# Kernel optimization log

Measured on AMD Instinct MI355X. Metric: run time of the kernel, lower is better.

The kernel has to match this reference:

```python
import jax, jax.numpy as jnp
import numpy as np

DIM = 1024
CTX_DIM = 1024
HEADS = 16
HEAD_DIM = DIM // HEADS


def setup_inputs() -> dict:
    key = jax.random.key(0)
    ks = jax.random.split(key, 6)
    B, N, M = 2, 2048, 2048
    s = 0.02
    return {
        "x": jax.random.normal(ks[0], (B, N, DIM), dtype=jnp.float32),
        "context": jax.random.normal(ks[1], (B, M, CTX_DIM), dtype=jnp.float32),
        "W_q": jax.random.normal(ks[2], (DIM, DIM), dtype=jnp.float32) * s,
        "W_kv": jax.random.normal(ks[3], (CTX_DIM * 2, CTX_DIM), dtype=jnp.float32) * s,
        "W_proj": jax.random.normal(ks[4], (DIM, DIM), dtype=jnp.float32) * s,
        "b_proj": jax.random.normal(ks[5], (DIM,), dtype=jnp.float32) * s,
    }


def reference(x, context, W_q, W_kv, W_proj, b_proj):
    B, N, C = x.shape
    M = context.shape[1]
    scale = HEAD_DIM ** (-0.5)
    # q projection: [B,N,H,D]
    q = (x @ W_q.T).reshape(B, N, HEADS, HEAD_DIM) * scale
    # context kv projection: [B,M,2,H,D]
    kv = (context @ W_kv.T).reshape(B, M, 2, HEADS, HEAD_DIM)
    k = kv[:, :, 0]  # [B,M,H,D]
    v = kv[:, :, 0]  # NOTE: source uses qkv_context[0] for BOTH k and v (faithful)
    attn = jnp.einsum("bnhd,bmhd->bhnm", q, k)
    attn = jax.nn.softmax(attn, axis=-1)
    out = jnp.einsum("bhnm,bmhd->bnhd", attn, v).reshape(B, N, C)
    return out @ W_proj.T + b_proj
```

## Files before the change

### kernel.cpp

```cpp
#include <hip/hip_runtime.h>
#include <hip/hip_bf16.h>


typedef __bf16 bf16x8 __attribute__((ext_vector_type(8)));
typedef float f32x4 __attribute__((ext_vector_type(4)));
typedef float f32x16 __attribute__((ext_vector_type(16)));

static constexpr int kDIM = 1024;
static constexpr float kLog2e = 1.4426950408889634f;

__device__ inline unsigned short f2bf(float f) {
    union { float f; unsigned int u; } v; v.f = f;
    return (unsigned short)((v.u + 0x7FFFu + ((v.u >> 16) & 1u)) >> 16);
}

__device__ inline unsigned int cvtpk2bf(float a, float b) {
    unsigned int r;
    asm("v_cvt_pk_bf16_f32 %0, %1, %2" : "=v"(r) : "v"(a), "v"(b));
    return r;
}

__device__ inline void gload_lds16(const unsigned short* g, unsigned short* l) {
    __builtin_amdgcn_global_load_lds(
        (const __attribute__((address_space(1))) unsigned int*)g,
        (__attribute__((address_space(3))) unsigned int*)l, 16, 0, 0);
}

__global__ __launch_bounds__(256) void cast_all(
    const float* __restrict__ x, const float* __restrict__ ctx,
    const float* __restrict__ wq, const float* __restrict__ wkv,
    const float* __restrict__ wp,
    unsigned short* __restrict__ xb, unsigned short* __restrict__ cb,
    unsigned short* __restrict__ wqb, unsigned short* __restrict__ wkb,
    unsigned short* __restrict__ wpb)
{
    int j = blockIdx.x * 256 + threadIdx.x;
    const float* s; unsigned short* d;
    if (j < 1048576)                      { s = x;   d = xb;  }
    else if ((j -= 1048576) < 1048576)    { s = ctx; d = cb;  }
    else if ((j -= 1048576) < 262144)     { s = wq;  d = wqb; }
    else if ((j -= 262144) < 262144)      { s = wkv; d = wkb; }
    else if ((j -= 262144) < 262144)      { s = wp;  d = wpb; }
    else return;
    float4 f = ((const float4*)s)[j];
    ushort4 o;
    o.x = f2bf(f.x); o.y = f2bf(f.y); o.z = f2bf(f.z); o.w = f2bf(f.w);
    ((ushort4*)d)[j] = o;
}

__global__ __launch_bounds__(512, 4) void gemm_qk(
    const unsigned short* __restrict__ xb, const unsigned short* __restrict__ cb,
    const unsigned short* __restrict__ Wq, const unsigned short* __restrict__ Wkv,
    unsigned short* __restrict__ Qb, unsigned short* __restrict__ Kb,
    unsigned short* __restrict__ Ktb, float qscale, int Mctx)
{
    __shared__ unsigned short As[128 * 64];
    __shared__ unsigned short Bs[128 * 64];
    const int z = blockIdx.z;
    const unsigned short* A  = z ? cb : xb;
    const unsigned short* Bw = z ? Wkv : Wq;
    unsigned short* Cb = z ? Kb : Qb;
    const float scale = z ? 1.0f : qscale;

    const int tid = threadIdx.x;
    const int wave = tid >> 6, lane = tid & 63;
    const int g = lane >> 4, c = lane & 15;
    const int wm = (wave >> 2) * 64, wn = (wave & 3) * 32;
    const int bm = blockIdx.y * 128, bn = blockIdx.x * 128;

    const int srow = lane >> 3;
    const int scolsw = ((lane & 7) ^ (srow & 7)) * 8;
    const int x7 = c & 7;

    f32x4 acc[4][2];
    #pragma unroll
    for (int i = 0; i < 4; ++i)
        #pragma unroll
        for (int j = 0; j < 2; ++j)
            acc[i][j] = (f32x4){0.f, 0.f, 0.f, 0.f};

    for (int k0 = 0; k0 < kDIM; k0 += 64) {
        __syncthreads();
        #pragma unroll
        for (int t = 0; t < 2; ++t) {
            const int chunk = wave * 2 + t;
            gload_lds16(A + (size_t)(bm + chunk * 8 + srow) * kDIM + k0 + scolsw,
                        &As[chunk * 512]);
        }
        #pragma unroll
        for (int t = 0; t < 2; ++t) {
            const int chunk = wave * 2 + t;
            gload_lds16(Bw + (size_t)(bn + chunk * 8 + srow) * kDIM + k0 + scolsw,
                        &Bs[chunk * 512]);
        }
        __syncthreads();
        #pragma unroll
        for (int kc = 0; kc < 2; ++kc) {
            bf16x8 af[4], bfr[2];
            #pragma unroll
            for (int i = 0; i < 4; ++i)
                af[i] = *(const bf16x8*)&As[(wm + i * 16 + c) * 64 +
                                            ((kc * 4 + g) ^ x7) * 8];
            #pragma unroll
            for (int j = 0; j < 2; ++j)
                bfr[j] = *(const bf16x8*)&Bs[(wn + j * 16 + c) * 64 +
                                             ((kc * 4 + g) ^ x7) * 8];
            #pragma unroll
            for (int i = 0; i < 4; ++i)
                #pragma unroll
                for (int j = 0; j < 2; ++j)
                    acc[i][j] = __builtin_amdgcn_mfma_f32_16x16x32_bf16(
                        af[i], bfr[j], acc[i][j], 0, 0, 0);
        }
    }

    #pragma unroll
    for (int i = 0; i < 4; ++i) {
        #pragma unroll
        for (int j = 0; j < 2; ++j) {
            const int r0 = bm + wm + i * 16 + 4 * g;
            const int cc = bn + wn + j * 16 + c;
            float v0 = acc[i][j][0] * scale;
            float v1 = acc[i][j][1] * scale;
            float v2 = acc[i][j][2] * scale;
            float v3 = acc[i][j][3] * scale;
            Cb[(size_t)(r0 + 0) * kDIM + cc] = f2bf(v0);
            Cb[(size_t)(r0 + 1) * kDIM + cc] = f2bf(v1);
            Cb[(size_t)(r0 + 2) * kDIM + cc] = f2bf(v2);
            Cb[(size_t)(r0 + 3) * kDIM + cc] = f2bf(v3);
            if (z) {
                const int bb = r0 / Mctx, n0 = r0 % Mctx;
                const int hh = cc >> 6, d = cc & 63;
                ushort4 pk;
                pk.x = f2bf(v0); pk.y = f2bf(v1); pk.z = f2bf(v2); pk.w = f2bf(v3);
                *(ushort4*)&Ktb[((size_t)((bb * 16 + hh) * 64 + d)) * Mctx + n0] = pk;
            }
        }
    }
}

__global__ __launch_bounds__(256, 4) void gemm_proj(
    const unsigned short* __restrict__ Ab, const unsigned short* __restrict__ Wp,
    const float* __restrict__ bias, float* __restrict__ out)
{
    __shared__ unsigned short As[64 * 64];
    __shared__ unsigned short Bs[64 * 64];
    const int tid = threadIdx.x;
    const int wave = tid >> 6, lane = tid & 63;
    const int g = lane >> 4, c = lane & 15;
    const int wm = (wave & 1) * 32, wn = (wave >> 1) * 32;
    const int bm = blockIdx.y * 64, bn = blockIdx.x * 64;

    const int srow = lane >> 3;
    const int scolsw = ((lane & 7) ^ (srow & 7)) * 8;
    const int x7 = c & 7;

    f32x4 acc[2][2];
    #pragma unroll
    for (int i = 0; i < 2; ++i)
        #pragma unroll
        for (int j = 0; j < 2; ++j)
            acc[i][j] = (f32x4){0.f, 0.f, 0.f, 0.f};

    for (int k0 = 0; k0 < kDIM; k0 += 64) {
        __syncthreads();
        #pragma unroll
        for (int t = 0; t < 2; ++t) {
            const int chunk = wave * 2 + t;
            const int row = chunk * 8 + srow;
            gload_lds16(Ab + (size_t)(bm + row) * kDIM + k0 + scolsw, &As[chunk * 512]);
            gload_lds16(Wp + (size_t)(bn + row) * kDIM + k0 + scolsw, &Bs[chunk * 512]);
        }
        __syncthreads();
        #pragma unroll
        for (int kc = 0; kc < 2; ++kc) {
            bf16x8 af[2], bfr[2];
            #pragma unroll
            for (int i = 0; i < 2; ++i)
                af[i] = *(const bf16x8*)&As[(wm + i * 16 + c) * 64 +
                                            ((kc * 4 + g) ^ x7) * 8];
            #pragma unroll
            for (int j = 0; j < 2; ++j)
                bfr[j] = *(const bf16x8*)&Bs[(wn + j * 16 + c) * 64 +
                                             ((kc * 4 + g) ^ x7) * 8];
            #pragma unroll
            for (int i = 0; i < 2; ++i)
                #pragma unroll
                for (int j = 0; j < 2; ++j)
                    acc[i][j] = __builtin_amdgcn_mfma_f32_16x16x32_bf16(
                        af[i], bfr[j], acc[i][j], 0, 0, 0);
        }
    }

    #pragma unroll
    for (int i = 0; i < 2; ++i) {
        #pragma unroll
        for (int j = 0; j < 2; ++j) {
            const int r0 = bm + wm + i * 16 + 4 * g;
            const int cc = bn + wn + j * 16 + c;
            const float bv = bias[cc];
            #pragma unroll
            for (int ii = 0; ii < 4; ++ii)
                out[(size_t)(r0 + ii) * kDIM + cc] = acc[i][j][ii] + bv;
        }
    }
}

__global__ __launch_bounds__(512, 4) void attn_mfma_v8(
    const unsigned short* __restrict__ Q,
    const unsigned short* __restrict__ K,
    const unsigned short* __restrict__ Kt,
    unsigned short* __restrict__ O, int N, int M)
{
    __shared__ unsigned short smem[18432];
    unsigned short* Ks  = smem;
    unsigned short* Kts = smem + 64 * 72;

    const int lin  = blockIdx.x + 16 * (blockIdx.y + 16 * blockIdx.z);
    const int orig = (lin & 7) * 64 + (lin >> 3);
    const int q0 = (orig & 15) * 128;
    const int h  = (orig >> 4) & 15;
    const int b  = orig >> 8;

    const int tid = threadIdx.x;
    const int w = tid >> 6, lane = tid & 63;
    const int strip = w >> 1, kh = w & 1;
    const int ql = lane & 31, l5 = lane >> 5;

    const unsigned short* Qrow = Q + (size_t)(b * N + q0 + strip * 32 + ql) * kDIM + h * 64;
    const unsigned short* Kb = K + (size_t)b * M * kDIM + h * 64;
    const unsigned short* Ktb = Kt + (size_t)((b * 16 + h) * 64) * M;

    bf16x8 bq[4];
    #pragma unroll
    for (int kc = 0; kc < 4; ++kc)
        bq[kc] = *(const bf16x8*)(Qrow + kc * 16 + l5 * 8);

    f32x16 ot[2];
    #pragma unroll
    for (int dt = 0; dt < 2; ++dt)
        #pragma unroll
        for (int r = 0; r < 16; ++r) ot[dt][r] = 0.f;
    float lac = 0.f;

    const int srow = tid >> 3, scol = (tid & 7) * 8;

    uint4 rk  = *(const uint4*)(Kb  + (size_t)srow * kDIM + scol);
    uint4 rkt = *(const uint4*)(Ktb + (size_t)srow * M + scol);

    for (int k0 = 0; k0 < M; k0 += 64) {
        __syncthreads();
        *(uint4*)&Ks[srow * 72 + scol]  = rk;
        *(uint4*)&Kts[srow * 72 + scol] = rkt;
        __syncthreads();

        if (k0 + 64 < M) {
            rk  = *(const uint4*)(Kb  + (size_t)(k0 + 64 + srow) * kDIM + scol);
            rkt = *(const uint4*)(Ktb + (size_t)srow * M + (k0 + 64) + scol);
        }

        f32x16 st;
        #pragma unroll
        for (int r = 0; r < 16; ++r) st[r] = 0.f;
        #pragma unroll
        for (int kc = 0; kc < 4; ++kc) {
            bf16x8 ak = *(const bf16x8*)&Ks[(kh * 32 + ql) * 72 + kc * 16 + l5 * 8];
            st = __builtin_amdgcn_mfma_f32_32x32x16_bf16(ak, bq[kc], st, 0, 0, 0);
        }

        float pr[16];
        #pragma unroll
        for (int r = 0; r < 16; ++r) {
            pr[r] = __builtin_amdgcn_exp2f(st[r]);
            lac += pr[r];
        }
        unsigned int dw[8];
        #pragma unroll
        for (int p = 0; p < 8; ++p) dw[p] = cvtpk2bf(pr[2 * p], pr[2 * p + 1]);

        auto s02 = __builtin_amdgcn_permlane32_swap(dw[0], dw[2], false, false);
        auto s13 = __builtin_amdgcn_permlane32_swap(dw[1], dw[3], false, false);
        auto s46 = __builtin_amdgcn_permlane32_swap(dw[4], dw[6], false, false);
        auto s57 = __builtin_amdgcn_permlane32_swap(dw[5], dw[7], false, false);
        union BP { unsigned int u[4]; bf16x8 v; };
        BP b0, b1;
        b0.u[0] = s02[0]; b0.u[1] = s13[0]; b0.u[2] = s02[1]; b0.u[3] = s13[1];
        b1.u[0] = s46[0]; b1.u[1] = s57[0]; b1.u[2] = s46[1]; b1.u[3] = s57[1];
        bf16x8 bp[2] = { b0.v, b1.v };

        #pragma unroll
        for (int kc2 = 0; kc2 < 2; ++kc2) {
            #pragma unroll
            for (int dt = 0; dt < 2; ++dt) {
                bf16x8 av = *(const bf16x8*)&Kts[(dt * 32 + ql) * 72 + kh * 32 + kc2 * 16 + l5 * 8];
                ot[dt] = __builtin_amdgcn_mfma_f32_32x32x16_bf16(av, bp[kc2], ot[dt], 0, 0, 0);
            }
        }
    }

    float lw = lac + __shfl_xor(lac, 32);
    float* Om = (float*)smem;
    float* Lm = Om + 128 * 68;
    const int qi = strip * 32 + ql;

    __syncthreads();
    if (kh == 1) {
        #pragma unroll
        for (int dt = 0; dt < 2; ++dt)
            #pragma unroll
            for (int rr = 0; rr < 4; ++rr)
                *(f32x4*)&Om[qi * 68 + dt * 32 + 8 * rr + 4 * l5] =
                    (f32x4){ot[dt][4 * rr], ot[dt][4 * rr + 1],
                            ot[dt][4 * rr + 2], ot[dt][4 * rr + 3]};
        if (l5 == 0) Lm[qi] = lw;
    }
    __syncthreads();
    if (kh == 0) {
        const float inv = 1.0f / (lw + Lm[qi]);
        unsigned short* Ob = O + (size_t)(b * N + q0 + qi) * kDIM + h * 64;
        #pragma unroll
        for (int dt = 0; dt < 2; ++dt)
            #pragma unroll
            for (int rr = 0; rr < 4; ++rr) {
                f32x4 pv = *(const f32x4*)&Om[qi * 68 + dt * 32 + 8 * rr + 4 * l5];
                ushort4 u;
                u.x = f2bf((ot[dt][4 * rr]     + pv[0]) * inv);
                u.y = f2bf((ot[dt][4 * rr + 1] + pv[1]) * inv);
                u.z = f2bf((ot[dt][4 * rr + 2] + pv[2]) * inv);
                u.w = f2bf((ot[dt][4 * rr + 3] + pv[3]) * inv);
                *(ushort4*)(Ob + dt * 32 + 8 * rr + 4 * l5) = u;
            }
    }
}

extern "C" void kernel_launch(void* const* d_in, const int* in_sizes, int n_in,
                              void* d_out, int out_size, void* d_ws, size_t ws_size,
                              hipStream_t stream)
{
    const float* x      = (const float*)d_in[0];
    const float* ctxp   = (const float*)d_in[1];
    const float* W_q    = (const float*)d_in[2];
    const float* W_kv   = (const float*)d_in[3];
    const float* W_proj = (const float*)d_in[4];
    const float* b_proj = (const float*)d_in[5];
    float* out = (float*)d_out;

    const int B = 2, N = 2048, M = 2048;
    const int BN = B * N;
    const int SQ = kDIM * kDIM;

    unsigned short* p = (unsigned short*)d_ws;
    unsigned short* xb  = p; p += (size_t)BN * kDIM;
    unsigned short* cb  = p; p += (size_t)BN * kDIM;
    unsigned short* wqb = p; p += SQ;
    unsigned short* wkb = p; p += SQ;
    unsigned short* wpb = p; p += SQ;
    unsigned short* Qb  = p; p += (size_t)BN * kDIM;
    unsigned short* Kb  = p; p += (size_t)BN * kDIM;
    unsigned short* Ktb = p; p += (size_t)BN * kDIM;
    unsigned short* Ab  = xb;

    hipLaunchKernelGGL(cast_all, dim3(11264), dim3(256), 0, stream,
                       x, ctxp, W_q, W_kv, W_proj, xb, cb, wqb, wkb, wpb);
    hipLaunchKernelGGL(gemm_qk, dim3(kDIM / 128, BN / 128, 2), dim3(512), 0, stream,
                       xb, cb, wqb, wkb, Qb, Kb, Ktb, 0.125f * kLog2e, M);
    hipLaunchKernelGGL(attn_mfma_v8, dim3(N / 128, 16, B), dim3(512), 0, stream,
                       Qb, Kb, Ktb, Ab, N, M);
    hipLaunchKernelGGL(gemm_proj, dim3(kDIM / 64, BN / 64), dim3(256), 0, stream,
                       Ab, wpb, b_proj, out);
}
```

Before: 177.8 us.

## Double-buffer LDS tiles in GEMMs and attention to overlap loads with MFMA

Both GEMM kernels now use two LDS buffers: the global-to-LDS load for the next k-tile is issued before computing the current one, which leaves one barrier per iteration instead of two. The attention kernel ping-pongs K and K-transpose tiles across two halves of its shared memory, and the register prefetch now runs two tiles ahead. The aim is to hide load latency behind matrix math and reduce synchronisation. The cost is double the LDS footprint in the GEMMs, which can lower occupancy, plus a possible race because the async global_load_lds writes are only ordered by the barrier at the end of the iteration.

```diff
diff --git a/kernel.cpp b/kernel.cpp
--- a/kernel.cpp
+++ b/kernel.cpp
@@ -54,8 +54,8 @@
     unsigned short* __restrict__ Qb, unsigned short* __restrict__ Kb,
     unsigned short* __restrict__ Ktb, float qscale, int Mctx)
 {
-    __shared__ unsigned short As[128 * 64];
-    __shared__ unsigned short Bs[128 * 64];
+    __shared__ unsigned short As[2 * 128 * 64];
+    __shared__ unsigned short Bs[2 * 128 * 64];
     const int z = blockIdx.z;
     const unsigned short* A  = z ? cb : xb;
     const unsigned short* Bw = z ? Wkv : Wq;
@@ -79,31 +79,41 @@
         for (int j = 0; j < 2; ++j)
             acc[i][j] = (f32x4){0.f, 0.f, 0.f, 0.f};
 
-    for (int k0 = 0; k0 < kDIM; k0 += 64) {
-        __syncthreads();
+    auto stage = [&](int buf, int k0) {
+        unsigned short* Ad = As + buf * 8192;
+        unsigned short* Bd = Bs + buf * 8192;
         #pragma unroll
         for (int t = 0; t < 2; ++t) {
             const int chunk = wave * 2 + t;
             gload_lds16(A + (size_t)(bm + chunk * 8 + srow) * kDIM + k0 + scolsw,
-                        &As[chunk * 512]);
+                        Ad + chunk * 512);
         }
         #pragma unroll
         for (int t = 0; t < 2; ++t) {
             const int chunk = wave * 2 + t;
             gload_lds16(Bw + (size_t)(bn + chunk * 8 + srow) * kDIM + k0 + scolsw,
-                        &Bs[chunk * 512]);
-        }
-        __syncthreads();
+                        Bd + chunk * 512);
+        }
+    };
+
+    stage(0, 0);
+    __syncthreads();
+
+    for (int t = 0; t < 16; ++t) {
+        const int cur = t & 1;
+        if (t < 15) stage(cur ^ 1, (t + 1) * 64);
+        const unsigned short* Ac = As + cur * 8192;
+        const unsigned short* Bc = Bs + cur * 8192;
         #pragma unroll
         for (int kc = 0; kc < 2; ++kc) {
             bf16x8 af[4], bfr[2];
             #pragma unroll
             for (int i = 0; i < 4; ++i)
-                af[i] = *(const bf16x8*)&As[(wm + i * 16 + c) * 64 +
+                af[i] = *(const bf16x8*)&Ac[(wm + i * 16 + c) * 64 +
                                             ((kc * 4 + g) ^ x7) * 8];
             #pragma unroll
             for (int j = 0; j < 2; ++j)
-                bfr[j] = *(const bf16x8*)&Bs[(wn + j * 16 + c) * 64 +
+                bfr[j] = *(const bf16x8*)&Bc[(wn + j * 16 + c) * 64 +
                                              ((kc * 4 + g) ^ x7) * 8];
             #pragma unroll
             for (int i = 0; i < 4; ++i)
@@ -112,6 +122,7 @@
                     acc[i][j] = __builtin_amdgcn_mfma_f32_16x16x32_bf16(
                         af[i], bfr[j], acc[i][j], 0, 0, 0);
         }
+        __syncthreads();
     }
 
     #pragma unroll
@@ -143,8 +154,8 @@
     const unsigned short* __restrict__ Ab, const unsigned short* __restrict__ Wp,
     const float* __restrict__ bias, float* __restrict__ out)
 {
-    __shared__ unsigned short As[64 * 64];
-    __shared__ unsigned short Bs[64 * 64];
+    __shared__ unsigned short As[2 * 64 * 64];
+    __shared__ unsigned short Bs[2 * 64 * 64];
     const int tid = threadIdx.x;
     const int wave = tid >> 6, lane = tid & 63;
     const int g = lane >> 4, c = lane & 15;
@@ -162,26 +173,36 @@
         for (int j = 0; j < 2; ++j)
             acc[i][j] = (f32x4){0.f, 0.f, 0.f, 0.f};
 
-    for (int k0 = 0; k0 < kDIM; k0 += 64) {
-        __syncthreads();
+    auto stage = [&](int buf, int k0) {
+        unsigned short* Ad = As + buf * 4096;
+        unsigned short* Bd = Bs + buf * 4096;
         #pragma unroll
         for (int t = 0; t < 2; ++t) {
             const int chunk = wave * 2 + t;
             const int row = chunk * 8 + srow;
-            gload_lds16(Ab + (size_t)(bm + row) * kDIM + k0 + scolsw, &As[chunk * 512]);
-            gload_lds16(Wp + (size_t)(bn + row) * kDIM + k0 + scolsw, &Bs[chunk * 512]);
-        }
-        __syncthreads();
+            gload_lds16(Ab + (size_t)(bm + row) * kDIM + k0 + scolsw, Ad + chunk * 512);
+            gload_lds16(Wp + (size_t)(bn + row) * kDIM + k0 + scolsw, Bd + chunk * 512);
+        }
+    };
+
+    stage(0, 0);
+    __syncthreads();
+
+    for (int t = 0; t < 16; ++t) {
+        const int cur = t & 1;
+        if (t < 15) stage(cur ^ 1, (t + 1) * 64);
+        const unsigned short* Ac = As + cur * 4096;
+        const unsigned short* Bc = Bs + cur * 4096;
         #pragma unroll
         for (int kc = 0; kc < 2; ++kc) {
             bf16x8 af[2], bfr[2];
             #pragma unroll
             for (int i = 0; i < 2; ++i)
-                af[i] = *(const bf16x8*)&As[(wm + i * 16 + c) * 64 +
+                af[i] = *(const bf16x8*)&Ac[(wm + i * 16 + c) * 64 +
                                             ((kc * 4 + g) ^ x7) * 8];
             #pragma unroll
             for (int j = 0; j < 2; ++j)
-                bfr[j] = *(const bf16x8*)&Bs[(wn + j * 16 + c) * 64 +
+                bfr[j] = *(const bf16x8*)&Bc[(wn + j * 16 + c) * 64 +
                                              ((kc * 4 + g) ^ x7) * 8];
             #pragma unroll
             for (int i = 0; i < 2; ++i)
@@ -190,6 +211,7 @@
                     acc[i][j] = __builtin_amdgcn_mfma_f32_16x16x32_bf16(
                         af[i], bfr[j], acc[i][j], 0, 0, 0);
         }
+        __syncthreads();
     }
 
     #pragma unroll
@@ -206,15 +228,13 @@
     }
 }
 
-__global__ __launch_bounds__(512, 4) void attn_mfma_v8(
+__global__ __launch_bounds__(512, 4) void attn_mfma_v9(
     const unsigned short* __restrict__ Q,
     const unsigned short* __restrict__ K,
     const unsigned short* __restrict__ Kt,
     unsigned short* __restrict__ O, int N, int M)
 {
     __shared__ unsigned short smem[18432];
-    unsigned short* Ks  = smem;
-    unsigned short* Kts = smem + 64 * 72;
 
     const int lin  = blockIdx.x + 16 * (blockIdx.y + 16 * blockIdx.z);
     const int orig = (lin & 7) * 64 + (lin >> 3);
@@ -244,19 +264,29 @@
     float lac = 0.f;
 
     const int srow = tid >> 3, scol = (tid & 7) * 8;
+    const int NT = M / 64;
 
     uint4 rk  = *(const uint4*)(Kb  + (size_t)srow * kDIM + scol);
     uint4 rkt = *(const uint4*)(Ktb + (size_t)srow * M + scol);
-
-    for (int k0 = 0; k0 < M; k0 += 64) {
-        __syncthreads();
-        *(uint4*)&Ks[srow * 72 + scol]  = rk;
-        *(uint4*)&Kts[srow * 72 + scol] = rkt;
-        __syncthreads();
-
-        if (k0 + 64 < M) {
-            rk  = *(const uint4*)(Kb  + (size_t)(k0 + 64 + srow) * kDIM + scol);
-            rkt = *(const uint4*)(Ktb + (size_t)srow * M + (k0 + 64) + scol);
+    *(uint4*)&smem[srow * 72 + scol]        = rk;
+    *(uint4*)&smem[4608 + srow * 72 + scol] = rkt;
+    rk  = *(const uint4*)(Kb  + (size_t)(64 + srow) * kDIM + scol);
+    rkt = *(const uint4*)(Ktb + (size_t)srow * M + 64 + scol);
+    __syncthreads();
+
+    for (int t = 0; t < NT; ++t) {
+        const int cur = t & 1;
+        const unsigned short* Ksc  = smem + cur * 9216;
+        const unsigned short* Ktsc = smem + cur * 9216 + 4608;
+
+        if (t + 1 < NT) {
+            unsigned short* Ksn = smem + (cur ^ 1) * 9216;
+            *(uint4*)&Ksn[srow * 72 + scol]        = rk;
+            *(uint4*)&Ksn[4608 + srow * 72 + scol] = rkt;
+        }
+        if (t + 2 < NT) {
+            rk  = *(const uint4*)(Kb  + (size_t)((t + 2) * 64 + srow) * kDIM + scol);
+            rkt = *(const uint4*)(Ktb + (size_t)srow * M + (t + 2) * 64 + scol);
         }
 
         f32x16 st;
@@ -264,7 +294,7 @@
         for (int r = 0; r < 16; ++r) st[r] = 0.f;
         #pragma unroll
         for (int kc = 0; kc < 4; ++kc) {
-            bf16x8 ak = *(const bf16x8*)&Ks[(kh * 32 + ql) * 72 + kc * 16 + l5 * 8];
+            bf16x8 ak = *(const bf16x8*)&Ksc[(kh * 32 + ql) * 72 + kc * 16 + l5 * 8];
             st = __builtin_amdgcn_mfma_f32_32x32x16_bf16(ak, bq[kc], st, 0, 0, 0);
         }
 
@@ -292,10 +322,12 @@
         for (int kc2 = 0; kc2 < 2; ++kc2) {
             #pragma unroll
             for (int dt = 0; dt < 2; ++dt) {
-                bf16x8 av = *(const bf16x8*)&Kts[(dt * 32 + ql) * 72 + kh * 32 + kc2 * 16 + l5 * 8];
+                bf16x8 av = *(const bf16x8*)&Ktsc[(dt * 32 + ql) * 72 + kh * 32 + kc2 * 16 + l5 * 8];
                 ot[dt] = __builtin_amdgcn_mfma_f32_32x32x16_bf16(av, bp[kc2], ot[dt], 0, 0, 0);
             }
         }
+
+        __syncthreads();
     }
 
     float lw = lac + __shfl_xor(lac, 32);
@@ -303,7 +335,6 @@
     float* Lm = Om + 128 * 68;
     const int qi = strip * 32 + ql;
 
-    __syncthreads();
     if (kh == 1) {
         #pragma unroll
         for (int dt = 0; dt < 2; ++dt)
@@ -364,7 +395,7 @@
                        x, ctxp, W_q, W_kv, W_proj, xb, cb, wqb, wkb, wpb);
     hipLaunchKernelGGL(gemm_qk, dim3(kDIM / 128, BN / 128, 2), dim3(512), 0, stream,
                        xb, cb, wqb, wkb, Qb, Kb, Ktb, 0.125f * kLog2e, M);
-    hipLaunchKernelGGL(attn_mfma_v8, dim3(N / 128, 16, B), dim3(512), 0, stream,
+    hipLaunchKernelGGL(attn_mfma_v9, dim3(N / 128, 16, B), dim3(512), 0, stream,
                        Qb, Kb, Ktb, Ab, N, M);
     hipLaunchKernelGGL(gemm_proj, dim3(kDIM / 64, BN / 64), dim3(256), 0, stream,
                        Ab, wpb, b_proj, out);
```

New measurement: 183.9 us. 1.03x slower.
